# Optimization experiments

Measured on AMD Instinct MI355X. Metric: run time of the kernel, lower is better.

Reference implementation:

```python
import jax, jax.numpy as jnp
import numpy as np

N, T, D_FEAT, H = 8192, 60, 6, 64
NEG_SLOPE = 0.01  # torch LeakyReLU default


def setup_inputs() -> dict:
    key = jax.random.key(0)
    ks = jax.random.split(key, 20)
    s = lambda k, shape, fan: jax.random.normal(k, shape, jnp.float32) * (1.0 / np.sqrt(fan))
    inp = {
        'x': jax.random.normal(ks[0], (N, T, D_FEAT), jnp.float32),
        # LSTM layer 0 (input D_FEAT) and layer 1 (input H); gate order i,f,g,o
        'Wih0': s(ks[1], (4 * H, D_FEAT), H), 'Whh0': s(ks[2], (4 * H, H), H),
        'bih0': s(ks[3], (4 * H,), H), 'bhh0': s(ks[4], (4 * H,), H),
        'Wih1': s(ks[5], (4 * H, H), H), 'Whh1': s(ks[6], (4 * H, H), H),
        'bih1': s(ks[7], (4 * H,), H), 'bhh1': s(ks[8], (4 * H,), H),
        # GAT layer: transformation Linear(H,H) and attention vector a [2H,1] (randn in torch)
        'Wt': s(ks[9], (H, H), H), 'bt': s(ks[10], (H,), H),
        'a': jax.random.normal(ks[11], (2 * H, 1), jnp.float32),
        # fc and fc_out
        'Wfc': s(ks[12], (H, H), H), 'bfc': s(ks[13], (H,), H),
        'Wout': s(ks[14], (1, H), H), 'bout': s(ks[15], (1,), H),
    }
    return inp


def _lstm_layer(x, Wih, Whh, bih, bhh):
    # x: [N, T, Din] -> outputs [N, T, H]
    xg = jnp.einsum('ntd,gd->ntg', x, Wih) + bih + bhh  # precompute input gates

    def step(carry, xt):
        h, c = carry
        gates = xt + h @ Whh.T  # [N, 4H]
        i, f, g, o = jnp.split(gates, 4, axis=-1)
        c = jax.nn.sigmoid(f) * c + jax.nn.sigmoid(i) * jnp.tanh(g)
        h = jax.nn.sigmoid(o) * jnp.tanh(c)
        return (h, c), h

    n = x.shape[0]
    h0 = jnp.zeros((n, Whh.shape[1]), x.dtype)
    (_, _), hs = jax.lax.scan(step, (h0, h0), jnp.swapaxes(xg, 0, 1))
    return jnp.swapaxes(hs, 0, 1)


def _gat_layer(x, Wt, bt, a):
    # att[i,j] = leaky_relu(a1 . Wx_j + a2 . Wx_i); softmax over j; out = att @ x
    h = x @ Wt.T + bt                    # [N, H]
    hdim = h.shape[1]
    s1 = (h @ a[:hdim]).squeeze(-1)      # a1 . Wx_j  -> column term
    s2 = (h @ a[hdim:]).squeeze(-1)      # a2 . Wx_i  -> row term
    scores = jax.nn.leaky_relu(s2[:, None] + s1[None, :], NEG_SLOPE)  # [N, N]
    att = jax.nn.softmax(scores, axis=1)
    return att @ x


def reference(x, Wih0, Whh0, bih0, bhh0, Wih1, Whh1, bih1, bhh1,
              Wt, bt, a, Wfc, bfc, Wout, bout):
    out = _lstm_layer(x, Wih0, Whh0, bih0, bhh0)
    out = _lstm_layer(out, Wih1, Whh1, bih1, bhh1)
    last = out[:, -1, :]                 # [N, H]
    hidden = _gat_layer(last, Wt, bt, a) + last  # num_layers_gat = 1
    hidden = jax.nn.leaky_relu(hidden @ Wfc.T + bfc, NEG_SLOPE)
    return (hidden @ Wout.T + bout).squeeze(-1)  # [N]
```

## Files before the change

kernel.cpp:

```cpp
#include <hip/hip_runtime.h>

#define NN 8192
#define TT 60
#define DF 6
#define HH 64
#define GG 256
#define RS 132
#define CH 32
#define NB 256

typedef _Float16 half8 __attribute__((ext_vector_type(8)));
typedef float f32x4 __attribute__((ext_vector_type(4)));
#define MFMA16(a, b, c) __builtin_amdgcn_mfma_f32_16x16x32_f16((a), (b), (c), 0, 0, 0)

__device__ __forceinline__ float sigmoidf_(float x) {
    return __builtin_amdgcn_rcpf(1.0f + __expf(-x));
}
__device__ __forceinline__ float tanhf_(float x) {
    return __builtin_fmaf(2.0f, __builtin_amdgcn_rcpf(1.0f + __expf(-2.0f * x)), -1.0f);
}
__device__ __forceinline__ float lrelu_(float x) { return x > 0.0f ? x : 0.01f * x; }

__device__ __forceinline__ half8 ldw8(const float* __restrict__ p) {
    const float4* q = (const float4*)p;
    float4 u = q[0], v = q[1];
    half8 r;
    r[0]=(_Float16)u.x; r[1]=(_Float16)u.y; r[2]=(_Float16)u.z; r[3]=(_Float16)u.w;
    r[4]=(_Float16)v.x; r[5]=(_Float16)v.y; r[6]=(_Float16)v.z; r[7]=(_Float16)v.w;
    return r;
}

#define SXW (TT * 8 + 8)

__global__ __launch_bounds__(512, 4)
void lstm_fused_kernel(const float* __restrict__ x,
                       const float* __restrict__ Wih0, const float* __restrict__ Whh0,
                       const float* __restrict__ bih0, const float* __restrict__ bhh0,
                       const float* __restrict__ Wih1, const float* __restrict__ Whh1,
                       const float* __restrict__ bih1, const float* __restrict__ bhh1,
                       const float* __restrict__ Wt, const float* __restrict__ bt,
                       const float* __restrict__ av,
                       float* __restrict__ last_out,
                       float* __restrict__ s1g, float* __restrict__ s2g)
{
    __shared__ _Float16 sxp[16][SXW];
    __shared__ _Float16 h0buf[2][16][72];
    __shared__ _Float16 h1buf[2][16][72];
    __shared__ _Float16 zero16[8];
    __shared__ float sv1[HH], sv2[HH], sc12[2];

    const int tid  = threadIdx.x;
    const int w    = tid >> 6;
    const int grp  = w >> 2;
    const int cg   = w & 3;
    const int lane = tid & 63;
    const int quad = lane >> 4;
    const int l15  = lane & 15;
    const int hc   = cg * 16 + l15;
    const int n0   = blockIdx.x * 16;

    for (int i = tid; i < 16 * SXW / 2; i += 512) ((unsigned*)sxp)[i] = 0u;
    for (int i = tid; i < 2 * 16 * 72 / 2; i += 512) ((unsigned*)h0buf)[i] = 0u;
    for (int i = tid; i < 2 * 16 * 72 / 2; i += 512) ((unsigned*)h1buf)[i] = 0u;
    if (tid < 4) ((unsigned*)zero16)[tid] = 0u;
    __syncthreads();

    for (int idx = tid; idx < 16 * TT * DF; idx += 512) {
        const int m = idx / (TT * DF);
        const int r = idx - m * (TT * DF);
        const int t = r / DF;
        const int d = r - t * DF;
        sxp[m][t * 8 + d] = (_Float16)x[(size_t)(n0 + m) * (TT * DF) + r];
    }

    if (tid < HH) {
        float a1 = 0.f, a2 = 0.f;
        #pragma unroll 8
        for (int h = 0; h < HH; h++) {
            const float wt = Wt[h * HH + tid];
            a1 += wt * av[h];
            a2 += wt * av[HH + h];
        }
        sv1[tid] = a1; sv2[tid] = a2;
    } else if (tid == 64 || tid == 65) {
        const float* ap = av + (tid - 64) * HH;
        float c = 0.f;
        #pragma unroll 8
        for (int h = 0; h < HH; h++) c += bt[h] * ap[h];
        sc12[tid - 64] = c;
    }

    half8 wA[4][2], wB[4][2];
    float bias[4];
    half8 hzero;
    #pragma unroll
    for (int j = 0; j < 8; j++) hzero[j] = (_Float16)0.f;

    if (grp == 0) {
        #pragma unroll
        for (int nt = 0; nt < 4; nt++) {
            const int g = nt * 64 + hc;
            wA[nt][0] = ldw8(Whh0 + (size_t)g * HH + quad * 8);
            wA[nt][1] = ldw8(Whh0 + (size_t)g * HH + 32 + quad * 8);
            bias[nt]  = bih0[g] + bhh0[g];
            half8 t = hzero;
            if (quad == 0) {
                #pragma unroll
                for (int j = 0; j < DF; j++) t[j] = (_Float16)Wih0[g * DF + j];
            }
            wB[nt][0] = t;
            wB[nt][1] = hzero;
        }
    } else {
        #pragma unroll
        for (int nt = 0; nt < 4; nt++) {
            const int g = nt * 64 + hc;
            wA[nt][0] = ldw8(Wih1 + (size_t)g * HH + quad * 8);
            wA[nt][1] = ldw8(Wih1 + (size_t)g * HH + 32 + quad * 8);
            wB[nt][0] = ldw8(Whh1 + (size_t)g * HH + quad * 8);
            wB[nt][1] = ldw8(Whh1 + (size_t)g * HH + 32 + quad * 8);
            bias[nt]  = bih1[g] + bhh1[g];
        }
    }

    float cs[4] = {0.f, 0.f, 0.f, 0.f};
    __syncthreads();

    for (int i = 0; i <= TT; i++) {
        const int p = i & 1;
        if (grp == 0) {
            if (i < TT) {
                const half8 a0 = *(const half8*)&h0buf[p][l15][quad * 8];
                const half8 a1 = *(const half8*)&h0buf[p][l15][32 + quad * 8];
                const _Float16* xap = (quad == 0) ? &sxp[l15][i * 8] : zero16;
                const half8 ax = *(const half8*)xap;
                f32x4 gv[4];
                #pragma unroll
                for (int nt = 0; nt < 4; nt++) {
                    f32x4 c; c[0] = bias[nt]; c[1] = bias[nt]; c[2] = bias[nt]; c[3] = bias[nt];
                    c = MFMA16(ax, wB[nt][0], c);
                    c = MFMA16(a0, wA[nt][0], c);
                    c = MFMA16(a1, wA[nt][1], c);
                    gv[nt] = c;
                }
                _Float16 (*h0w)[72] = h0buf[p ^ 1];
                #pragma unroll
                for (int reg = 0; reg < 4; reg++) {
                    const float gi = gv[0][reg], gf = gv[1][reg], gc = gv[2][reg], go = gv[3][reg];
                    const float cc = sigmoidf_(gf) * cs[reg] + sigmoidf_(gi) * tanhf_(gc);
                    cs[reg] = cc;
                    h0w[quad * 4 + reg][hc] = (_Float16)(sigmoidf_(go) * tanhf_(cc));
                }
            }
        } else {
            if (i > 0) {
                const half8 a00 = *(const half8*)&h0buf[p][l15][quad * 8];
                const half8 a01 = *(const half8*)&h0buf[p][l15][32 + quad * 8];
                const half8 a10 = *(const half8*)&h1buf[p][l15][quad * 8];
                const half8 a11 = *(const half8*)&h1buf[p][l15][32 + quad * 8];
                f32x4 gv[4];
                #pragma unroll
                for (int nt = 0; nt < 4; nt++) {
                    f32x4 c; c[0] = bias[nt]; c[1] = bias[nt]; c[2] = bias[nt]; c[3] = bias[nt];
                    c = MFMA16(a00, wA[nt][0], c);
                    c = MFMA16(a01, wA[nt][1], c);
                    c = MFMA16(a10, wB[nt][0], c);
                    c = MFMA16(a11, wB[nt][1], c);
                    gv[nt] = c;
                }
                _Float16 (*h1w)[72] = h1buf[p ^ 1];
                #pragma unroll
                for (int reg = 0; reg < 4; reg++) {
                    const float gi = gv[0][reg], gf = gv[1][reg], gc = gv[2][reg], go = gv[3][reg];
                    const float cc = sigmoidf_(gf) * cs[reg] + sigmoidf_(gi) * tanhf_(gc);
                    cs[reg] = cc;
                    const float hv = sigmoidf_(go) * tanhf_(cc);
                    h1w[quad * 4 + reg][hc] = (_Float16)hv;
                    if (i == TT) last_out[(size_t)(n0 + quad * 4 + reg) * HH + hc] = hv;
                }
            }
        }
        __syncthreads();
    }

    {
        const _Float16 (*hf)[72] = h1buf[1];
        const int r  = tid >> 5;
        const int c0 = tid & 31;
        const float h1a = (float)hf[r][c0];
        const float h1b = (float)hf[r][c0 + 32];
        float p1 = h1a * sv1[c0] + h1b * sv1[c0 + 32];
        float p2 = h1a * sv2[c0] + h1b * sv2[c0 + 32];
        #pragma unroll
        for (int off = 16; off > 0; off >>= 1) {
            p1 += __shfl_xor(p1, off);
            p2 += __shfl_xor(p2, off);
        }
        if (c0 == 0) {
            s1g[n0 + r] = p1 + sc12[0];
            s2g[n0 + r] = p2 + sc12[1];
        }
    }
}

__global__ __launch_bounds__(256)
void rankfac_kernel(const float* __restrict__ s1g, const float* __restrict__ s2g,
                    float* __restrict__ Z, float* __restrict__ Ai, float* __restrict__ Bi,
                    float* __restrict__ U, float* __restrict__ W,
                    int* __restrict__ iperm, float* __restrict__ sortedD)
{
    __shared__ float sb[NN];
    __shared__ float sred[256];
    __shared__ int   sRank[32];
    const int tid = threadIdx.x;
    const int b   = blockIdx.x;
    const int j0  = b * 32;

    for (int idx = tid; idx < NN; idx += 256) sb[idx] = s1g[idx];
    if (tid < 32) sRank[tid] = 0;
    __syncthreads();

    float m = -1e30f;
    for (int idx = tid; idx < NN; idx += 256) m = fmaxf(m, sb[idx]);
    sred[tid] = m;
    __syncthreads();
    for (int s = 128; s > 0; s >>= 1) {
        if (tid < s) sred[tid] = fmaxf(sred[tid], sred[tid + s]);
        __syncthreads();
    }
    const float s1max = sred[0];

    if (tid < 32) {
        const int j = j0 + tid;
        const float z  = s2g[j] + s1max;
        const float mi = lrelu_(z);
        Z[j]  = z;
        Ai[j] = __expf(z - mi);
        Bi[j] = __expf(0.01f * z - mi);
        const float d = sb[j] - s1max;
        U[j] = __expf(d);
        W[j] = __expf(0.01f * d);
    }
    {
        const int jl = tid & 31;
        const int part = tid >> 5;
        const float sj = sb[j0 + jl];
        const int jg = j0 + jl;
        int cnt = 0;
        const int k0 = part * (NN / 8);
        #pragma unroll 4
        for (int k = k0; k < k0 + NN / 8; k++) {
            const float sk = sb[k];
            cnt += (sk < sj || (sk == sj && k < jg)) ? 1 : 0;
        }
        atomicAdd(&sRank[jl], cnt);
    }
    __syncthreads();
    if (tid < 32) {
        const int r = sRank[tid];
        iperm[r] = j0 + tid;
        sortedD[r] = sb[j0 + tid] - s1max;
    }
}

__global__ __launch_bounds__(256)
void scanA_kernel(const float* __restrict__ last, const float* __restrict__ U,
                  const float* __restrict__ W, const int* __restrict__ iperm,
                  float* __restrict__ chunkSum)
{
    __shared__ int   sj[CH];
    __shared__ float su[CH], sw[CH];
    __shared__ float al[CH][HH], bl[CH][HH];
    const int tid = threadIdx.x;
    const int b   = blockIdx.x;
    if (tid < CH) {
        const int j = iperm[b * CH + tid];
        sj[tid] = j; su[tid] = U[j]; sw[tid] = W[j];
    }
    __syncthreads();
    for (int idx = tid; idx < CH * HH; idx += 256) {
        const int rr = idx >> 6, c = idx & 63;
        const float lv = last[(size_t)sj[rr] * HH + c];
        al[rr][c] = su[rr] * lv;
        bl[rr][c] = sw[rr] * lv;
    }
    __syncthreads();
    if (tid < 130) {
        const int c = tid;
        float s = 0.f;
        if (c < 64) {
            for (int rr = 0; rr < CH; rr++) s += al[rr][c];
        } else if (c < 128) {
            for (int rr = 0; rr < CH; rr++) s += bl[rr][c - 64];
        } else if (c == 128) {
            for (int rr = 0; rr < CH; rr++) s += su[rr];
        } else {
            for (int rr = 0; rr < CH; rr++) s += sw[rr];
        }
        chunkSum[b * RS + c] = s;
    }
}

__global__ __launch_bounds__(256)
void scanB_kernel(const float* __restrict__ chunkSum, float* __restrict__ chunkOfs)
{
    __shared__ float wt[4];
    const int c   = blockIdx.x;
    const bool rev = (c < 64) || (c == 128);
    const int tid = threadIdx.x;
    const int lane = tid & 63, wv = tid >> 6;
    const int idx = rev ? (NB - 1 - tid) : tid;
    const float orig = chunkSum[idx * RS + c];
    float v = orig;
    #pragma unroll
    for (int d = 1; d < 64; d <<= 1) {
        const float t = __shfl_up(v, d);
        if (lane >= d) v += t;
    }
    if (lane == 63) wt[wv] = v;
    __syncthreads();
    float off = 0.f;
    for (int q = 0; q < wv; q++) off += wt[q];
    chunkOfs[idx * RS + c] = v + off - orig;
}

__global__ __launch_bounds__(256)
void scanC_kernel(const float* __restrict__ last, const float* __restrict__ U,
                  const float* __restrict__ W, const int* __restrict__ iperm,
                  const float* __restrict__ chunkOfs, float* __restrict__ PP)
{
    __shared__ int   sj[CH];
    __shared__ float su[CH], sw[CH];
    __shared__ float al[CH][HH], bl[CH][HH];
    const int tid = threadIdx.x;
    const int b   = blockIdx.x;
    if (tid < CH) {
        const int j = iperm[b * CH + tid];
        sj[tid] = j; su[tid] = U[j]; sw[tid] = W[j];
    }
    __syncthreads();
    for (int idx = tid; idx < CH * HH; idx += 256) {
        const int rr = idx >> 6, c = idx & 63;
        const float lv = last[(size_t)sj[rr] * HH + c];
        al[rr][c] = su[rr] * lv;
        bl[rr][c] = sw[rr] * lv;
    }
    __syncthreads();
    if (tid < 130) {
        const int c = tid;
        const bool rev = (c < 64) || (c == 128);
        float run = chunkOfs[b * RS + c];
        if (rev) {
            if (b == NB - 1) PP[(size_t)NN * RS + c] = 0.f;
            for (int rr = CH - 1; rr >= 0; rr--) {
                const float val = (c < 64) ? al[rr][c] : su[rr];
                run += val;
                PP[(size_t)(b * CH + rr) * RS + c] = run;
            }
        } else {
            for (int rr = 0; rr < CH; rr++) {
                PP[(size_t)(b * CH + rr) * RS + c] = run;
                run += (c < 128) ? bl[rr][c - 64] : sw[rr];
            }
            if (b == NB - 1) PP[(size_t)NN * RS + c] = run;
        }
    }
}

__global__ __launch_bounds__(256)
void applyfc_kernel(const float* __restrict__ last,
                    const float* __restrict__ Z, const float* __restrict__ Ai, const float* __restrict__ Bi,
                    const float* __restrict__ sortedD, const float* __restrict__ PP,
                    const float* __restrict__ Wfc, const float* __restrict__ bfc,
                    const float* __restrict__ Wout, const float* __restrict__ bout,
                    float* __restrict__ out)
{
    __shared__ float sdD[NN];
    __shared__ float sW[HH][HH + 1];
    __shared__ float sbF[HH], saF[HH];
    const int tid = threadIdx.x;
    for (int idx = tid; idx < NN; idx += 256) sdD[idx] = sortedD[idx];
    for (int idx = tid; idx < HH * HH; idx += 256) {
        const int h = idx >> 6, d = idx & 63;
        sW[d][h] = Wfc[idx];
    }
    if (tid < HH) { sbF[tid] = bfc[tid]; saF[tid] = Wout[tid]; }
    __syncthreads();

    const int wv = tid >> 6, lane = tid & 63;
    const int i0 = blockIdx.x * 32 + wv * 8;
    float zi[8]; int lo[8], hi[8];
    #pragma unroll
    for (int q = 0; q < 8; q++) { zi[q] = Z[i0 + q]; lo[q] = 0; hi[q] = NN; }
    for (int iter = 0; iter < 13; iter++) {
        #pragma unroll
        for (int q = 0; q < 8; q++) {
            if (lo[q] < hi[q]) {
                const int mid = (lo[q] + hi[q]) >> 1;
                const float dm = sdD[mid];
                if (zi[q] + dm > 0.f) hi[q] = mid; else lo[q] = mid + 1;
            }
        }
    }
    float gv[8];
    #pragma unroll
    for (int q = 0; q < 8; q++) {
        const int i = i0 + q;
        const float* rowp = PP + (size_t)lo[q] * RS;
        const float pu  = rowp[lane];
        const float pw  = rowp[64 + lane];
        const float pud = rowp[128];
        const float pwd = rowp[129];
        const float ai = Ai[i], bi = Bi[i];
        const float numer = bi * pw + ai * pu;
        const float den   = bi * pwd + ai * pud;
        const float lv = last[(size_t)i * HH + lane];
        gv[q] = numer * __builtin_amdgcn_rcpf(den) + lv;
    }
    const float bo = bout[0];
    #pragma unroll
    for (int q = 0; q < 8; q++) {
        float acc = sbF[lane];
        #pragma unroll
        for (int d = 0; d < HH; d++) acc += __shfl(gv[q], d) * sW[d][lane];
        float prod = lrelu_(acc) * saF[lane];
        #pragma unroll
        for (int off = 32; off > 0; off >>= 1) prod += __shfl_xor(prod, off);
        if (lane == 0) out[i0 + q] = prod + bo;
    }
}

extern "C" void kernel_launch(void* const* d_in, const int* in_sizes, int n_in,
                              void* d_out, int out_size, void* d_ws, size_t ws_size,
                              hipStream_t stream)
{
    (void)in_sizes; (void)n_in; (void)out_size; (void)ws_size;
    const float* x    = (const float*)d_in[0];
    const float* Wih0 = (const float*)d_in[1];
    const float* Whh0 = (const float*)d_in[2];
    const float* bih0 = (const float*)d_in[3];
    const float* bhh0 = (const float*)d_in[4];
    const float* Wih1 = (const float*)d_in[5];
    const float* Whh1 = (const float*)d_in[6];
    const float* bih1 = (const float*)d_in[7];
    const float* bhh1 = (const float*)d_in[8];
    const float* Wt   = (const float*)d_in[9];
    const float* bt   = (const float*)d_in[10];
    const float* a    = (const float*)d_in[11];
    const float* Wfc  = (const float*)d_in[12];
    const float* bfc  = (const float*)d_in[13];
    const float* Wout = (const float*)d_in[14];
    const float* bout = (const float*)d_in[15];
    float* out = (float*)d_out;

    float* ws       = (float*)d_ws;
    float* last     = ws;
    float* s1g      = last + (size_t)NN*HH;
    float* s2g      = s1g + NN;
    float* Z        = s2g + NN;
    float* Ai       = Z + NN;
    float* Bi       = Ai + NN;
    float* U        = Bi + NN;
    float* W        = U + NN;
    float* sortedD  = W + NN;
    int*   iperm    = (int*)(sortedD + NN);
    float* chunkSum = (float*)(iperm + NN);
    float* chunkOfs = chunkSum + NB*RS;
    float* PP       = chunkOfs + NB*RS;

    lstm_fused_kernel<<<dim3(NN / 16), dim3(512), 0, stream>>>(
        x, Wih0, Whh0, bih0, bhh0, Wih1, Whh1, bih1, bhh1,
        Wt, bt, a, last, s1g, s2g);
    rankfac_kernel<<<dim3(NB), dim3(256), 0, stream>>>(
        s1g, s2g, Z, Ai, Bi, U, W, iperm, sortedD);
    scanA_kernel<<<dim3(NB), dim3(256), 0, stream>>>(last, U, W, iperm, chunkSum);
    scanB_kernel<<<dim3(130), dim3(256), 0, stream>>>(chunkSum, chunkOfs);
    scanC_kernel<<<dim3(NB), dim3(256), 0, stream>>>(last, U, W, iperm, chunkOfs, PP);
    applyfc_kernel<<<dim3(NB), dim3(256), 0, stream>>>(
        last, Z, Ai, Bi, sortedD, PP, Wfc, bfc, Wout, bout, out);
}
```

Baseline: 261.9 us.

## Duplicate LSTM MFMA across wave pairs and fuse gate activations with exp2

The block grows from 8 to 16 waves. Each pair of waves computes the same MFMA gate tiles redundantly, and each wave handles the activations for only two of the four accumulator rows, halving the serial transcendental work per wave on every timestep. The sigmoid and tanh chain is also fused into a combined form that uses exp2 with shared reciprocals, so fewer rcp instructions are issued. The cost is duplicated MFMA work, heavier barriers with 1024 threads, and an occupancy change from the new launch bounds. The clamped exp2 form may differ slightly in numerics.

```diff
diff --git a/kernel.cpp b/kernel.cpp
--- a/kernel.cpp
+++ b/kernel.cpp
@@ -13,13 +13,23 @@
 typedef float f32x4 __attribute__((ext_vector_type(4)));
 #define MFMA16(a, b, c) __builtin_amdgcn_mfma_f32_16x16x32_f16((a), (b), (c), 0, 0, 0)
 
-__device__ __forceinline__ float sigmoidf_(float x) {
-    return __builtin_amdgcn_rcpf(1.0f + __expf(-x));
-}
-__device__ __forceinline__ float tanhf_(float x) {
-    return __builtin_fmaf(2.0f, __builtin_amdgcn_rcpf(1.0f + __expf(-2.0f * x)), -1.0f);
-}
+#define LOG2E 1.44269504f
+
 __device__ __forceinline__ float lrelu_(float x) { return x > 0.0f ? x : 0.01f * x; }
+
+__device__ __forceinline__ void lstm_act2(float gi, float gf, float gg, float go,
+                                          float& c, float& h)
+{
+    const float ei = __builtin_amdgcn_exp2f(gi * -LOG2E);
+    const float ef = __builtin_amdgcn_exp2f(gf * -LOG2E);
+    const float eg = __builtin_amdgcn_exp2f(fminf(gg * (-2.f * LOG2E), 63.f));
+    const float sf = __builtin_amdgcn_rcpf(1.f + ef);
+    const float tg_si = (1.f - eg) * __builtin_amdgcn_rcpf((1.f + ei) * (1.f + eg));
+    c = __builtin_fmaf(sf, c, tg_si);
+    const float eo = __builtin_amdgcn_exp2f(go * -LOG2E);
+    const float ec = __builtin_amdgcn_exp2f(fminf(c * (-2.f * LOG2E), 63.f));
+    h = (1.f - ec) * __builtin_amdgcn_rcpf((1.f + eo) * (1.f + ec));
+}
 
 __device__ __forceinline__ half8 ldw8(const float* __restrict__ p) {
     const float4* q = (const float4*)p;
@@ -32,7 +42,7 @@
 
 #define SXW (TT * 8 + 8)
 
-__global__ __launch_bounds__(512, 4)
+__global__ __launch_bounds__(1024, 8)
 void lstm_fused_kernel(const float* __restrict__ x,
                        const float* __restrict__ Wih0, const float* __restrict__ Whh0,
                        const float* __restrict__ bih0, const float* __restrict__ bhh0,
@@ -51,21 +61,24 @@
 
     const int tid  = threadIdx.x;
     const int w    = tid >> 6;
-    const int grp  = w >> 2;
-    const int cg   = w & 3;
+    const int grp  = w >> 3;
+    const int sub  = w & 7;
+    const int cg   = sub >> 1;
+    const int pr   = sub & 1;
     const int lane = tid & 63;
     const int quad = lane >> 4;
     const int l15  = lane & 15;
     const int hc   = cg * 16 + l15;
     const int n0   = blockIdx.x * 16;
-
-    for (int i = tid; i < 16 * SXW / 2; i += 512) ((unsigned*)sxp)[i] = 0u;
-    for (int i = tid; i < 2 * 16 * 72 / 2; i += 512) ((unsigned*)h0buf)[i] = 0u;
-    for (int i = tid; i < 2 * 16 * 72 / 2; i += 512) ((unsigned*)h1buf)[i] = 0u;
+    const int r0   = pr * 2;
+
+    for (int i = tid; i < 16 * SXW / 2; i += 1024) ((unsigned*)sxp)[i] = 0u;
+    for (int i = tid; i < 2 * 16 * 72 / 2; i += 1024) ((unsigned*)h0buf)[i] = 0u;
+    for (int i = tid; i < 2 * 16 * 72 / 2; i += 1024) ((unsigned*)h1buf)[i] = 0u;
     if (tid < 4) ((unsigned*)zero16)[tid] = 0u;
     __syncthreads();
 
-    for (int idx = tid; idx < 16 * TT * DF; idx += 512) {
+    for (int idx = tid; idx < 16 * TT * DF; idx += 1024) {
         const int m = idx / (TT * DF);
         const int r = idx - m * (TT * DF);
         const int t = r / DF;
@@ -123,7 +136,7 @@
         }
     }
 
-    float cs[4] = {0.f, 0.f, 0.f, 0.f};
+    float cs0 = 0.f, cs1 = 0.f;
     __syncthreads();
 
     for (int i = 0; i <= TT; i++) {
@@ -143,14 +156,19 @@
                     c = MFMA16(a1, wA[nt][1], c);
                     gv[nt] = c;
                 }
+                float ga[4], gb[4];
+                #pragma unroll
+                for (int nt = 0; nt < 4; nt++) {
+                    ga[nt] = pr ? gv[nt][2] : gv[nt][0];
+                    gb[nt] = pr ? gv[nt][3] : gv[nt][1];
+                }
+                float hva, hvb;
+                lstm_act2(ga[0], ga[1], ga[2], ga[3], cs0, hva);
+                lstm_act2(gb[0], gb[1], gb[2], gb[3], cs1, hvb);
                 _Float16 (*h0w)[72] = h0buf[p ^ 1];
-                #pragma unroll
-                for (int reg = 0; reg < 4; reg++) {
-                    const float gi = gv[0][reg], gf = gv[1][reg], gc = gv[2][reg], go = gv[3][reg];
-                    const float cc = sigmoidf_(gf) * cs[reg] + sigmoidf_(gi) * tanhf_(gc);
-                    cs[reg] = cc;
-                    h0w[quad * 4 + reg][hc] = (_Float16)(sigmoidf_(go) * tanhf_(cc));
-                }
+                const int rw = quad * 4 + r0;
+                h0w[rw][hc]     = (_Float16)hva;
+                h0w[rw + 1][hc] = (_Float16)hvb;
             }
         } else {
             if (i > 0) {
@@ -168,22 +186,29 @@
                     c = MFMA16(a11, wB[nt][1], c);
                     gv[nt] = c;
                 }
+                float ga[4], gb[4];
+                #pragma unroll
+                for (int nt = 0; nt < 4; nt++) {
+                    ga[nt] = pr ? gv[nt][2] : gv[nt][0];
+                    gb[nt] = pr ? gv[nt][3] : gv[nt][1];
+                }
+                float hva, hvb;
+                lstm_act2(ga[0], ga[1], ga[2], ga[3], cs0, hva);
+                lstm_act2(gb[0], gb[1], gb[2], gb[3], cs1, hvb);
                 _Float16 (*h1w)[72] = h1buf[p ^ 1];
-                #pragma unroll
-                for (int reg = 0; reg < 4; reg++) {
-                    const float gi = gv[0][reg], gf = gv[1][reg], gc = gv[2][reg], go = gv[3][reg];
-                    const float cc = sigmoidf_(gf) * cs[reg] + sigmoidf_(gi) * tanhf_(gc);
-                    cs[reg] = cc;
-                    const float hv = sigmoidf_(go) * tanhf_(cc);
-                    h1w[quad * 4 + reg][hc] = (_Float16)hv;
-                    if (i == TT) last_out[(size_t)(n0 + quad * 4 + reg) * HH + hc] = hv;
+                const int rw = quad * 4 + r0;
+                h1w[rw][hc]     = (_Float16)hva;
+                h1w[rw + 1][hc] = (_Float16)hvb;
+                if (i == TT) {
+                    last_out[(size_t)(n0 + rw) * HH + hc]     = hva;
+                    last_out[(size_t)(n0 + rw + 1) * HH + hc] = hvb;
                 }
             }
         }
         __syncthreads();
     }
 
-    {
+    if (tid < 512) {
         const _Float16 (*hf)[72] = h1buf[1];
         const int r  = tid >> 5;
         const int c0 = tid & 31;
@@ -468,7 +493,7 @@
     float* chunkOfs = chunkSum + NB*RS;
     float* PP       = chunkOfs + NB*RS;
 
-    lstm_fused_kernel<<<dim3(NN / 16), dim3(512), 0, stream>>>(
+    lstm_fused_kernel<<<dim3(NN / 16), dim3(1024), 0, stream>>>(
         x, Wih0, Whh0, bih0, bhh0, Wih1, Whh1, bih1, bhh1,
         Wt, bt, a, last, s1g, s2g);
     rankfac_kernel<<<dim3(NB), dim3(256), 0, stream>>>(
```

New measurement: 957.4 us. 3.66x slower.
